# Performance work log

Measured on AMD Instinct MI355X. Metric: run time of the kernel, lower is better.

## Reference

```python
import jax, jax.numpy as jnp
import numpy as np

B, N, DIN, DOUT = 8, 2048, 128, 128

def setup_inputs() -> dict:
    key = jax.random.key(0)
    k1, k2, k3, k4 = jax.random.split(key, 4)
    x = jax.random.normal(k1, (B, N, DIN), dtype=jnp.float32)
    adj = jax.random.uniform(k2, (B, N, N), dtype=jnp.float32)
    W = jax.random.normal(k3, (DIN, DOUT), dtype=jnp.float32) / np.sqrt(DIN)
    b = jax.random.normal(k4, (DOUT,), dtype=jnp.float32) * 0.01
    return {"x": x, "adj": adj, "W": W, "b": b}

def reference(x, adj, W, b):
    # degree over last dim of adj: [B, N]
    degree = jnp.sum(adj, axis=2)
    d_norm = 1.0 / jnp.sqrt(degree + 1e-8)
    # D^{-1/2} A D^{-1/2} == row/col elementwise scaling (same math as diag_embed+bmm)
    adj_norm = d_norm[:, :, None] * adj * d_norm[:, None, :]
    support = jnp.einsum('bnm,bmd->bnd', adj_norm, x)  # [B, N, DIN]
    return support @ W + b  # [B, N, DOUT]
```

## Files before the change

kernel.cpp:

```cpp
#include <hip/hip_runtime.h>
#include <hip/hip_bf16.h>

#define NN 2048
#define DD 128

typedef __attribute__((ext_vector_type(4))) float f32x4;
typedef __attribute__((ext_vector_type(8))) short short8;

__device__ __forceinline__ unsigned short f2bf_bits(float f) {
  union { __hip_bfloat16 h; unsigned short s; } u;
  u.h = __float2bfloat16(f);
  return u.s;
}

__device__ __forceinline__ short8 cvt8(f32x4 a, f32x4 b) {
  short8 r;
  r[0] = (short)f2bf_bits(a[0]); r[1] = (short)f2bf_bits(a[1]);
  r[2] = (short)f2bf_bits(a[2]); r[3] = (short)f2bf_bits(a[3]);
  r[4] = (short)f2bf_bits(b[0]); r[5] = (short)f2bf_bits(b[1]);
  r[6] = (short)f2bf_bits(b[2]); r[7] = (short)f2bf_bits(b[3]);
  return r;
}

__device__ __forceinline__ void gld16(const void* src, void* lds) {
  __builtin_amdgcn_global_load_lds(
      (const __attribute__((address_space(1))) void*)src,
      (__attribute__((address_space(3))) void*)lds, 16, 0, 0);
}

__global__ void k_degree(const float* __restrict__ adj, float* __restrict__ dnorm) {
  const int wv = threadIdx.x >> 6;
  const int ln = threadIdx.x & 63;
  const int row = blockIdx.x * 4 + wv;
  const f32x4* rowp = (const f32x4*)(adj + (size_t)row * NN);
  float s = 0.0f;
#pragma unroll
  for (int i = 0; i < 8; ++i) {
    f32x4 v = rowp[i * 64 + ln];
    s += v[0] + v[1] + v[2] + v[3];
  }
#pragma unroll
  for (int off = 32; off >= 1; off >>= 1) s += __shfl_xor(s, off);
  if (ln == 0) dnorm[row] = rsqrtf(s + 1e-8f);
}

__global__ void k_y(const float* __restrict__ x, const float* __restrict__ W,
                    const float* __restrict__ dnorm, short* __restrict__ yT) {
  const int ln = threadIdx.x & 63;
  const int wv = threadIdx.x >> 6;
  const int bb = blockIdx.x >> 5;
  const int n0 = (blockIdx.x & 31) << 6;
  const int l15 = ln & 15, l4 = ln >> 4;
  const int dbase = wv * 32;

  short8 af[2][4];
#pragma unroll
  for (int dt = 0; dt < 2; ++dt)
#pragma unroll
    for (int ks = 0; ks < 4; ++ks) {
      short8 a;
#pragma unroll
      for (int j = 0; j < 8; ++j)
        a[j] = (short)f2bf_bits(W[(size_t)(ks * 32 + l4 * 8 + j) * DD + dbase + dt * 16 + l15]);
      af[dt][ks] = a;
    }

  f32x4 acc[2][4];
#pragma unroll
  for (int dt = 0; dt < 2; ++dt)
#pragma unroll
    for (int nt = 0; nt < 4; ++nt) acc[dt][nt] = (f32x4)0.0f;

  const float* xb = x + (size_t)bb * NN * DD;
  const float* dnb = dnorm + (size_t)bb * NN;
#pragma unroll
  for (int nt = 0; nt < 4; ++nt) {
    const int n = n0 + nt * 16 + l15;
    const float dn = dnb[n];
#pragma unroll
    for (int ks = 0; ks < 4; ++ks) {
      f32x4 p = *(const f32x4*)(xb + (size_t)n * DD + ks * 32 + l4 * 8);
      f32x4 q = *(const f32x4*)(xb + (size_t)n * DD + ks * 32 + l4 * 8 + 4);
      short8 bf = cvt8(p * dn, q * dn);
#pragma unroll
      for (int dt = 0; dt < 2; ++dt)
        acc[dt][nt] = __builtin_amdgcn_mfma_f32_16x16x32_bf16(af[dt][ks], bf, acc[dt][nt], 0, 0, 0);
    }
  }

  short* yb = yT + (size_t)bb * DD * NN;
#pragma unroll
  for (int dt = 0; dt < 2; ++dt)
#pragma unroll
    for (int nt = 0; nt < 4; ++nt)
#pragma unroll
      for (int rr = 0; rr < 4; ++rr) {
        int d = dbase + dt * 16 + l4 * 4 + rr;
        yb[(size_t)d * NN + n0 + nt * 16 + l15] = (short)f2bf_bits(acc[dt][nt][rr]);
      }
}

__launch_bounds__(512, 1)
__global__ void k_gemm2(const float* __restrict__ adj, const short* __restrict__ yT,
                        const float* __restrict__ dnorm, const float* __restrict__ bias,
                        float* __restrict__ out) {
  __shared__ float As[6][4096];

  const int t = threadIdx.x;
  const int ln = t & 63;
  const int wv = t >> 6;
  const int orig = ((blockIdx.x & 7) << 5) | (blockIdx.x >> 3);
  const int bb = orig >> 5;
  const int m0 = (orig & 31) << 6;

  const char* ablk = (const char*)(adj + ((size_t)bb * NN + m0) * NN);
  const int oc = (wv << 4) + (ln & 15);
  const int kg8 = (ln >> 4) << 3;
  const short* ybase = yT + ((size_t)bb * DD + oc) * NN;

  f32x4 acc[4];
#pragma unroll
  for (int m = 0; m < 4; ++m) acc[m] = (f32x4)0.0f;

  auto stage = [&](int tile, int buf) {
#pragma unroll
    for (int j = 0; j < 2; ++j) {
      unsigned L = ((unsigned)j << 13) + ((unsigned)t << 4);
      unsigned row = L >> 8;
      unsigned off = L & 255u;
      unsigned soff = off ^ ((row & 7u) << 4);
      const char* src = ablk + (size_t)row * (NN * 4) + (size_t)tile * 256 + soff;
      gld16(src, (char*)As + buf * 16384 + L);
    }
  };
  auto loadB = [&](int tile, int ks) -> short8 {
    return *(const short8*)(ybase + ((tile & 31) << 6) + ks * 32 + kg8);
  };
  auto compute = [&](int buf, short8 b0, short8 b1) {
    const char* base = (const char*)As + buf * 16384;
#pragma unroll
    for (int ks = 0; ks < 2; ++ks) {
      short8 bf = ks ? b1 : b0;
#pragma unroll
      for (int m = 0; m < 4; ++m) {
        unsigned row = (unsigned)(m * 16 + (ln & 15));
        unsigned c = (unsigned)(ks * 128 + (ln >> 4) * 32);
        unsigned sw = (row & 7u) << 4;
        f32x4 f0 = *(const f32x4*)(base + (row << 8) + (c ^ sw));
        f32x4 f1 = *(const f32x4*)(base + (row << 8) + ((c + 16) ^ sw));
        acc[m] = __builtin_amdgcn_mfma_f32_16x16x32_bf16(cvt8(f0, f1), bf, acc[m], 0, 0, 0);
      }
    }
  };

#pragma unroll
  for (int p = 0; p < 5; ++p) stage(p, p);
  short8 b0k0 = loadB(0, 0), b0k1 = loadB(0, 1);
  short8 b1k0 = loadB(1, 0), b1k1 = loadB(1, 1);
  asm volatile("s_waitcnt vmcnt(0)\n\ts_barrier" ::: "memory");

  int cbuf = 0, sbuf = 5;
#pragma unroll 1
  for (int tt = 0; tt < 32; tt += 2) {
    if (tt + 5 < 32) stage(tt + 5, sbuf);
    short8 n0k0 = loadB(tt + 2, 0), n0k1 = loadB(tt + 2, 1);
    compute(cbuf, b0k0, b0k1);
    asm volatile("s_waitcnt vmcnt(12)\n\ts_barrier" ::: "memory");
    cbuf = (cbuf == 5) ? 0 : cbuf + 1;
    sbuf = (sbuf == 5) ? 0 : sbuf + 1;
    if (tt + 6 < 32) stage(tt + 6, sbuf);
    short8 n1k0 = loadB(tt + 3, 0), n1k1 = loadB(tt + 3, 1);
    compute(cbuf, b1k0, b1k1);
    asm volatile("s_waitcnt vmcnt(12)\n\ts_barrier" ::: "memory");
    cbuf = (cbuf == 5) ? 0 : cbuf + 1;
    sbuf = (sbuf == 5) ? 0 : sbuf + 1;
    b0k0 = n0k0; b0k1 = n0k1; b1k0 = n1k0; b1k1 = n1k1;
  }

  const float bv = bias[oc];
  const int rbase = (ln >> 4) << 2;
#pragma unroll
  for (int m = 0; m < 4; ++m) {
    f32x4 dn = *(const f32x4*)(dnorm + (size_t)bb * NN + m0 + m * 16 + rbase);
#pragma unroll
    for (int rr = 0; rr < 4; ++rr)
      out[(size_t)(bb * NN + m0 + m * 16 + rbase + rr) * DD + oc] = acc[m][rr] * dn[rr] + bv;
  }
}

extern "C" void kernel_launch(void* const* d_in, const int* in_sizes, int n_in,
                              void* d_out, int out_size, void* d_ws, size_t ws_size,
                              hipStream_t stream) {
  (void)in_sizes; (void)n_in; (void)out_size; (void)ws_size;
  const float* x = (const float*)d_in[0];
  const float* adj = (const float*)d_in[1];
  const float* W = (const float*)d_in[2];
  const float* bias = (const float*)d_in[3];
  float* out = (float*)d_out;

  char* ws = (char*)d_ws;
  float* dnorm = (float*)ws;
  short* yT = (short*)(ws + (1 << 16));

  k_degree<<<4096, 256, 0, stream>>>(adj, dnorm);
  k_y<<<256, 256, 0, stream>>>(x, W, dnorm, yT);
  k_gemm2<<<256, 512, 0, stream>>>(adj, yT, dnorm, bias, out);
}
```

Measured before the change: 67.93 us.

## Shrink LDS ring to four stages with deeper B-register prefetch

```diff
diff --git a/kernel.cpp b/kernel.cpp
--- a/kernel.cpp
+++ b/kernel.cpp
@@ -104,7 +104,7 @@
 __global__ void k_gemm2(const float* __restrict__ adj, const short* __restrict__ yT,
                         const float* __restrict__ dnorm, const float* __restrict__ bias,
                         float* __restrict__ out) {
-  __shared__ float As[6][4096];
+  __shared__ float As[4][4096];
 
   const int t = threadIdx.x;
   const int ln = t & 63;
@@ -134,7 +134,7 @@
     }
   };
   auto loadB = [&](int tile, int ks) -> short8 {
-    return *(const short8*)(ybase + ((tile & 31) << 6) + ks * 32 + kg8);
+    return *(const short8*)(ybase + (tile << 6) + ks * 32 + kg8);
   };
   auto compute = [&](int buf, short8 b0, short8 b1) {
     const char* base = (const char*)As + buf * 16384;
@@ -153,29 +153,31 @@
     }
   };
 
-#pragma unroll
-  for (int p = 0; p < 5; ++p) stage(p, p);
-  short8 b0k0 = loadB(0, 0), b0k1 = loadB(0, 1);
-  short8 b1k0 = loadB(1, 0), b1k1 = loadB(1, 1);
+  stage(0, 0); stage(1, 1); stage(2, 2);
+  short8 p0k0 = loadB(0, 0), p0k1 = loadB(0, 1);
+  short8 p1k0 = loadB(1, 0), p1k1 = loadB(1, 1);
+  short8 p2k0 = loadB(2, 0), p2k1 = loadB(2, 1);
+  short8 p3k0 = loadB(3, 0), p3k1 = loadB(3, 1);
   asm volatile("s_waitcnt vmcnt(0)\n\ts_barrier" ::: "memory");
 
-  int cbuf = 0, sbuf = 5;
+#define GITER(T, PK0, PK1)                                              \
+  {                                                                     \
+    stage(((T) + 3) & 31, ((T) + 3) & 3);                               \
+    short8 nb0 = loadB(((T) + 4) & 31, 0);                              \
+    short8 nb1 = loadB(((T) + 4) & 31, 1);                              \
+    compute((T) & 3, PK0, PK1);                                         \
+    asm volatile("s_waitcnt vmcnt(10)\n\ts_barrier" ::: "memory");      \
+    PK0 = nb0; PK1 = nb1;                                               \
+  }
+
 #pragma unroll 1
-  for (int tt = 0; tt < 32; tt += 2) {
-    if (tt + 5 < 32) stage(tt + 5, sbuf);
-    short8 n0k0 = loadB(tt + 2, 0), n0k1 = loadB(tt + 2, 1);
-    compute(cbuf, b0k0, b0k1);
-    asm volatile("s_waitcnt vmcnt(12)\n\ts_barrier" ::: "memory");
-    cbuf = (cbuf == 5) ? 0 : cbuf + 1;
-    sbuf = (sbuf == 5) ? 0 : sbuf + 1;
-    if (tt + 6 < 32) stage(tt + 6, sbuf);
-    short8 n1k0 = loadB(tt + 3, 0), n1k1 = loadB(tt + 3, 1);
-    compute(cbuf, b1k0, b1k1);
-    asm volatile("s_waitcnt vmcnt(12)\n\ts_barrier" ::: "memory");
-    cbuf = (cbuf == 5) ? 0 : cbuf + 1;
-    sbuf = (sbuf == 5) ? 0 : sbuf + 1;
-    b0k0 = n0k0; b0k1 = n0k1; b1k0 = n1k0; b1k1 = n1k1;
-  }
+  for (int t4 = 0; t4 < 32; t4 += 4) {
+    GITER(t4 + 0, p0k0, p0k1);
+    GITER(t4 + 1, p1k0, p1k1);
+    GITER(t4 + 2, p2k0, p2k1);
+    GITER(t4 + 3, p3k0, p3k1);
+  }
+#undef GITER
 
   const float bv = bias[oc];
   const int rbase = (ln >> 4) << 2;
```

New measurement: 69.68 us. +2.6%, slower.

## Restructure adj GEMM so each wave owns 16 rows with per-wave LDS staging

Applied to the files above, without the earlier changes.

```diff
diff --git a/kernel.cpp b/kernel.cpp
--- a/kernel.cpp
+++ b/kernel.cpp
@@ -100,91 +100,102 @@
       }
 }
 
-__launch_bounds__(512, 1)
-__global__ void k_gemm2(const float* __restrict__ adj, const short* __restrict__ yT,
-                        const float* __restrict__ dnorm, const float* __restrict__ bias,
-                        float* __restrict__ out) {
-  __shared__ float As[6][4096];
+__launch_bounds__(256)
+__global__ void k_wgemm3(const float* __restrict__ adj, const short* __restrict__ yT,
+                         const float* __restrict__ dnorm, const float* __restrict__ bias,
+                         float* __restrict__ out) {
+  __shared__ char As[4][4][4096];
 
   const int t = threadIdx.x;
   const int ln = t & 63;
   const int wv = t >> 6;
+  const int l15 = ln & 15, l4 = ln >> 4;
   const int orig = ((blockIdx.x & 7) << 5) | (blockIdx.x >> 3);
   const int bb = orig >> 5;
-  const int m0 = (orig & 31) << 6;
-
-  const char* ablk = (const char*)(adj + ((size_t)bb * NN + m0) * NN);
-  const int oc = (wv << 4) + (ln & 15);
-  const int kg8 = (ln >> 4) << 3;
-  const short* ybase = yT + ((size_t)bb * DD + oc) * NN;
-
-  f32x4 acc[4];
-#pragma unroll
-  for (int m = 0; m < 4; ++m) acc[m] = (f32x4)0.0f;
-
-  auto stage = [&](int tile, int buf) {
-#pragma unroll
-    for (int j = 0; j < 2; ++j) {
-      unsigned L = ((unsigned)j << 13) + ((unsigned)t << 4);
+  const size_t rowbase = (size_t)bb * NN + ((size_t)(orig & 31) << 6) + (wv << 4);
+
+  const char* awave = (const char*)(adj + rowbase * NN);
+  char* ldsb = &As[wv][0][0];
+
+  const short* ybb = yT + (size_t)bb * DD * NN + (l4 << 3);
+  const short* bp[8];
+#pragma unroll
+  for (int c = 0; c < 8; ++c) bp[c] = ybb + (size_t)(c * 16 + l15) * NN;
+
+  f32x4 acc[8];
+#pragma unroll
+  for (int c = 0; c < 8; ++c) acc[c] = (f32x4)0.f;
+
+  auto stage = [&](int kt, int buf) {
+#pragma unroll
+    for (int j = 0; j < 4; ++j) {
+      unsigned L = ((unsigned)j << 10) + ((unsigned)ln << 4);
       unsigned row = L >> 8;
       unsigned off = L & 255u;
       unsigned soff = off ^ ((row & 7u) << 4);
-      const char* src = ablk + (size_t)row * (NN * 4) + (size_t)tile * 256 + soff;
-      gld16(src, (char*)As + buf * 16384 + L);
+      gld16(awave + (size_t)row * (NN * 4) + (size_t)kt * 256 + soff,
+            ldsb + (buf << 12) + L);
     }
   };
-  auto loadB = [&](int tile, int ks) -> short8 {
-    return *(const short8*)(ybase + ((tile & 31) << 6) + ks * 32 + kg8);
+  auto compute = [&](int buf, short8 B0[8], short8 B1[8]) {
+    const char* base = ldsb + (buf << 12);
+    const unsigned sw = ((unsigned)l15 & 7u) << 4;
+    const unsigned rowb = (unsigned)l15 << 8;
+#pragma unroll
+    for (int ks = 0; ks < 2; ++ks) {
+      unsigned o = (unsigned)(ks * 128 + l4 * 32);
+      f32x4 f0 = *(const f32x4*)(base + rowb + (o ^ sw));
+      f32x4 f1 = *(const f32x4*)(base + rowb + ((o + 16) ^ sw));
+      short8 af = cvt8(f0, f1);
+#pragma unroll
+      for (int c = 0; c < 8; ++c)
+        acc[c] = __builtin_amdgcn_mfma_f32_16x16x32_bf16(af, ks ? B1[c] : B0[c], acc[c], 0, 0, 0);
+    }
   };
-  auto compute = [&](int buf, short8 b0, short8 b1) {
-    const char* base = (const char*)As + buf * 16384;
-#pragma unroll
-    for (int ks = 0; ks < 2; ++ks) {
-      short8 bf = ks ? b1 : b0;
-#pragma unroll
-      for (int m = 0; m < 4; ++m) {
-        unsigned row = (unsigned)(m * 16 + (ln & 15));
-        unsigned c = (unsigned)(ks * 128 + (ln >> 4) * 32);
-        unsigned sw = (row & 7u) << 4;
-        f32x4 f0 = *(const f32x4*)(base + (row << 8) + (c ^ sw));
-        f32x4 f1 = *(const f32x4*)(base + (row << 8) + ((c + 16) ^ sw));
-        acc[m] = __builtin_amdgcn_mfma_f32_16x16x32_bf16(cvt8(f0, f1), bf, acc[m], 0, 0, 0);
+
+  short8 E0[8], E1[8], O0[8], O1[8];
+#pragma unroll
+  for (int c = 0; c < 8; ++c) {
+    E0[c] = *(const short8*)(bp[c]);
+    E1[c] = *(const short8*)(bp[c] + 32);
+  }
+  stage(0, 0);
+  stage(1, 1);
+  asm volatile("s_waitcnt vmcnt(0)" ::: "memory");
+
+#pragma unroll 1
+  for (int t2 = 0; t2 < 32; t2 += 2) {
+    {
+      const int bt = (t2 + 1) & 31;
+#pragma unroll
+      for (int c = 0; c < 8; ++c) {
+        O0[c] = *(const short8*)(bp[c] + bt * 64);
+        O1[c] = *(const short8*)(bp[c] + bt * 64 + 32);
       }
-    }
-  };
-
-#pragma unroll
-  for (int p = 0; p < 5; ++p) stage(p, p);
-  short8 b0k0 = loadB(0, 0), b0k1 = loadB(0, 1);
-  short8 b1k0 = loadB(1, 0), b1k1 = loadB(1, 1);
-  asm volatile("s_waitcnt vmcnt(0)\n\ts_barrier" ::: "memory");
-
-  int cbuf = 0, sbuf = 5;
-#pragma unroll 1
-  for (int tt = 0; tt < 32; tt += 2) {
-    if (tt + 5 < 32) stage(tt + 5, sbuf);
-    short8 n0k0 = loadB(tt + 2, 0), n0k1 = loadB(tt + 2, 1);
-    compute(cbuf, b0k0, b0k1);
-    asm volatile("s_waitcnt vmcnt(12)\n\ts_barrier" ::: "memory");
-    cbuf = (cbuf == 5) ? 0 : cbuf + 1;
-    sbuf = (sbuf == 5) ? 0 : sbuf + 1;
-    if (tt + 6 < 32) stage(tt + 6, sbuf);
-    short8 n1k0 = loadB(tt + 3, 0), n1k1 = loadB(tt + 3, 1);
-    compute(cbuf, b1k0, b1k1);
-    asm volatile("s_waitcnt vmcnt(12)\n\ts_barrier" ::: "memory");
-    cbuf = (cbuf == 5) ? 0 : cbuf + 1;
-    sbuf = (sbuf == 5) ? 0 : sbuf + 1;
-    b0k0 = n0k0; b0k1 = n0k1; b1k0 = n1k0; b1k1 = n1k1;
-  }
-
-  const float bv = bias[oc];
-  const int rbase = (ln >> 4) << 2;
-#pragma unroll
-  for (int m = 0; m < 4; ++m) {
-    f32x4 dn = *(const f32x4*)(dnorm + (size_t)bb * NN + m0 + m * 16 + rbase);
+      stage((t2 + 2) & 31, (t2 + 2) & 3);
+      asm volatile("s_waitcnt vmcnt(40)" ::: "memory");
+      compute(t2 & 3, E0, E1);
+    }
+    {
+      const int bt = (t2 + 2) & 31;
+#pragma unroll
+      for (int c = 0; c < 8; ++c) {
+        E0[c] = *(const short8*)(bp[c] + bt * 64);
+        E1[c] = *(const short8*)(bp[c] + bt * 64 + 32);
+      }
+      stage((t2 + 3) & 31, (t2 + 3) & 3);
+      asm volatile("s_waitcnt vmcnt(40)" ::: "memory");
+      compute((t2 + 1) & 3, O0, O1);
+    }
+  }
+
+  f32x4 dn4 = *(const f32x4*)(dnorm + rowbase + (l4 << 2));
+#pragma unroll
+  for (int c = 0; c < 8; ++c) {
+    const float bv = bias[c * 16 + l15];
 #pragma unroll
     for (int rr = 0; rr < 4; ++rr)
-      out[(size_t)(bb * NN + m0 + m * 16 + rbase + rr) * DD + oc] = acc[m][rr] * dn[rr] + bv;
+      out[(rowbase + (l4 << 2) + rr) * DD + c * 16 + l15] = acc[c][rr] * dn4[rr] + bv;
   }
 }
 
@@ -204,5 +215,5 @@
 
   k_degree<<<4096, 256, 0, stream>>>(adj, dnorm);
   k_y<<<256, 256, 0, stream>>>(x, W, dnorm, yT);
-  k_gemm2<<<256, 512, 0, stream>>>(adj, yT, dnorm, bias, out);
-}
+  k_wgemm3<<<256, 256, 0, stream>>>(adj, yT, dnorm, bias, out);
+}
```

Result: slower. 97.41 us (+43.4%).

## Restructure adj GEMM pipeline to double-buffered 256-column stages

Applied to the files above, without the earlier changes.

```diff
diff --git a/kernel.cpp b/kernel.cpp
--- a/kernel.cpp
+++ b/kernel.cpp
@@ -101,84 +101,79 @@
 }
 
 __launch_bounds__(512, 1)
-__global__ void k_gemm2(const float* __restrict__ adj, const short* __restrict__ yT,
+__global__ void k_gemm4(const float* __restrict__ adj, const short* __restrict__ yT,
                         const float* __restrict__ dnorm, const float* __restrict__ bias,
                         float* __restrict__ out) {
-  __shared__ float As[6][4096];
+  __shared__ char As[2][65536];
 
   const int t = threadIdx.x;
   const int ln = t & 63;
   const int wv = t >> 6;
+  const int l15 = ln & 15, l4 = ln >> 4;
   const int orig = ((blockIdx.x & 7) << 5) | (blockIdx.x >> 3);
   const int bb = orig >> 5;
   const int m0 = (orig & 31) << 6;
 
   const char* ablk = (const char*)(adj + ((size_t)bb * NN + m0) * NN);
-  const int oc = (wv << 4) + (ln & 15);
-  const int kg8 = (ln >> 4) << 3;
+  const int oc = (wv << 4) + l15;
+  const int kg8 = l4 << 3;
   const short* ybase = yT + ((size_t)bb * DD + oc) * NN;
 
   f32x4 acc[4];
 #pragma unroll
   for (int m = 0; m < 4; ++m) acc[m] = (f32x4)0.0f;
 
-  auto stage = [&](int tile, int buf) {
-#pragma unroll
-    for (int j = 0; j < 2; ++j) {
-      unsigned L = ((unsigned)j << 13) + ((unsigned)t << 4);
-      unsigned row = L >> 8;
-      unsigned off = L & 255u;
-      unsigned soff = off ^ ((row & 7u) << 4);
-      const char* src = ablk + (size_t)row * (NN * 4) + (size_t)tile * 256 + soff;
-      gld16(src, (char*)As + buf * 16384 + L);
+  auto stage = [&](int S, int buf) {
+#pragma unroll
+    for (int i = 0; i < 8; ++i) {
+      const int row = (wv << 3) + i;
+      const char* src = ablk + (size_t)row * (NN * 4) + (size_t)S * 1024 +
+                        (((unsigned)(ln ^ (i & 7))) << 4);
+      gld16(src, (char*)As + (buf << 16) + ((unsigned)row << 10));
     }
   };
-  auto loadB = [&](int tile, int ks) -> short8 {
-    return *(const short8*)(ybase + ((tile & 31) << 6) + ks * 32 + kg8);
+  auto loadB = [&](int S, short8 B[8]) {
+#pragma unroll
+    for (int kk = 0; kk < 8; ++kk)
+      B[kk] = *(const short8*)(ybase + S * 256 + kk * 32 + kg8);
   };
-  auto compute = [&](int buf, short8 b0, short8 b1) {
-    const char* base = (const char*)As + buf * 16384;
-#pragma unroll
-    for (int ks = 0; ks < 2; ++ks) {
-      short8 bf = ks ? b1 : b0;
+  auto compute = [&](int buf, short8 B[8]) {
+    const char* base = (const char*)As + (buf << 16);
+#pragma unroll
+    for (int kk = 0; kk < 8; ++kk) {
 #pragma unroll
       for (int m = 0; m < 4; ++m) {
-        unsigned row = (unsigned)(m * 16 + (ln & 15));
-        unsigned c = (unsigned)(ks * 128 + (ln >> 4) * 32);
-        unsigned sw = (row & 7u) << 4;
-        f32x4 f0 = *(const f32x4*)(base + (row << 8) + (c ^ sw));
-        f32x4 f1 = *(const f32x4*)(base + (row << 8) + ((c + 16) ^ sw));
-        acc[m] = __builtin_amdgcn_mfma_f32_16x16x32_bf16(cvt8(f0, f1), bf, acc[m], 0, 0, 0);
+        const unsigned row = (unsigned)(m * 16 + l15);
+        const unsigned s = row & 7u;
+        const unsigned q0 = (unsigned)(kk * 8 + l4 * 2);
+        f32x4 f0 = *(const f32x4*)(base + (row << 10) + ((q0 ^ s) << 4));
+        f32x4 f1 = *(const f32x4*)(base + (row << 10) + (((q0 + 1) ^ s) << 4));
+        acc[m] = __builtin_amdgcn_mfma_f32_16x16x32_bf16(cvt8(f0, f1), B[kk], acc[m], 0, 0, 0);
       }
     }
   };
 
-#pragma unroll
-  for (int p = 0; p < 5; ++p) stage(p, p);
-  short8 b0k0 = loadB(0, 0), b0k1 = loadB(0, 1);
-  short8 b1k0 = loadB(1, 0), b1k1 = loadB(1, 1);
+  short8 E[8], O[8];
+  stage(0, 0);
+  loadB(0, E);
   asm volatile("s_waitcnt vmcnt(0)\n\ts_barrier" ::: "memory");
 
-  int cbuf = 0, sbuf = 5;
 #pragma unroll 1
-  for (int tt = 0; tt < 32; tt += 2) {
-    if (tt + 5 < 32) stage(tt + 5, sbuf);
-    short8 n0k0 = loadB(tt + 2, 0), n0k1 = loadB(tt + 2, 1);
-    compute(cbuf, b0k0, b0k1);
-    asm volatile("s_waitcnt vmcnt(12)\n\ts_barrier" ::: "memory");
-    cbuf = (cbuf == 5) ? 0 : cbuf + 1;
-    sbuf = (sbuf == 5) ? 0 : sbuf + 1;
-    if (tt + 6 < 32) stage(tt + 6, sbuf);
-    short8 n1k0 = loadB(tt + 3, 0), n1k1 = loadB(tt + 3, 1);
-    compute(cbuf, b1k0, b1k1);
-    asm volatile("s_waitcnt vmcnt(12)\n\ts_barrier" ::: "memory");
-    cbuf = (cbuf == 5) ? 0 : cbuf + 1;
-    sbuf = (sbuf == 5) ? 0 : sbuf + 1;
-    b0k0 = n0k0; b0k1 = n0k1; b1k0 = n1k0; b1k1 = n1k1;
+  for (int S2 = 0; S2 < 8; S2 += 2) {
+    if (S2 + 1 < 8) { stage(S2 + 1, (S2 + 1) & 1); loadB(S2 + 1, O); }
+    compute(S2 & 1, E);
+    if (S2 + 1 < 8)
+      asm volatile("s_waitcnt vmcnt(8)\n\ts_barrier" ::: "memory");
+    if (S2 + 1 < 8) {
+      if (S2 + 2 < 8) { stage(S2 + 2, (S2 + 2) & 1); loadB(S2 + 2, E); }
+      compute((S2 + 1) & 1, O);
+      if (S2 + 2 < 8)
+        asm volatile("s_waitcnt vmcnt(8)\n\ts_barrier" ::: "memory");
+    }
   }
 
   const float bv = bias[oc];
-  const int rbase = (ln >> 4) << 2;
+  const int rbase = l4 << 2;
 #pragma unroll
   for (int m = 0; m < 4; ++m) {
     f32x4 dn = *(const f32x4*)(dnorm + (size_t)bb * NN + m0 + m * 16 + rbase);
@@ -204,5 +199,5 @@
 
   k_degree<<<4096, 256, 0, stream>>>(adj, dnorm);
   k_y<<<256, 256, 0, stream>>>(x, W, dnorm, yT);
-  k_gemm2<<<256, 512, 0, stream>>>(adj, yT, dnorm, bias, out);
-}
+  k_gemm4<<<256, 512, 0, stream>>>(adj, yT, dnorm, bias, out);
+}
```

Result: no change. 67.32 us (-0.9%).
